# Performance work log

Hardware: AMD Instinct MI355X
Metric: run time of the kernel (lower is better)

Reference implementation:

```python
import jax, jax.numpy as jnp
import numpy as np

# The 8 structuring elements from the torch module, in order.
_KERNELS = np.array([
    [[1.,1.,1.],[1.,1.,1.],[1.,1.,1.]],
    [[0.,1.,1.],[0.,1.,1.],[0.,1.,1.]],
    [[1.,1.,1.],[1.,1.,1.],[0.,0.,0.]],
    [[0.,0.,0.],[0.,1.,1.],[0.,1.,1.]],
    [[0.,1.,0.],[0.,1.,0.],[0.,1.,0.]],
    [[0.,0.,0.],[1.,1.,1.],[0.,0.,0.]],
    [[0.,1.,0.],[0.,1.,0.],[0.,0.,0.]],
    [[0.,0.,0.],[1.,1.,0.],[0.,0.,0.]],
], dtype=np.float32)


def _conv3x3(x, k):
    # x: [N,1,H,W], k: [3,3] -> same-padded single-channel conv (cross-correlation, like torch conv2d)
    return jax.lax.conv_general_dilated(
        x, k[None, None, :, :], window_strides=(1, 1),
        padding=((1, 1), (1, 1)),
        dimension_numbers=('NCHW', 'OIHW', 'NCHW'))


def setup_inputs() -> dict:
    key = jax.random.key(0)
    N, H, W = 16, 1024, 1024
    x = (jax.random.uniform(key, (N, 1, H, W)) < 0.5).astype(jnp.float32)
    kernels = jnp.asarray(_KERNELS)  # [8,3,3]
    return {"x": x, "kernels": kernels}


def reference(x, kernels):
    output = jnp.zeros_like(x)
    # Sequential loop over the 8 fixed structuring elements (data dependency on x).
    for i in range(8):
        k = kernels[i]
        eroded = _conv3x3(x, k)
        ksum = jnp.sum(k)
        mask = (eroded >= ksum).astype(x.dtype)
        output = jnp.maximum(output, mask)
        # mark(): dilate the mask with the flipped binarized kernel
        dil_k = jnp.flip((k > 0).astype(x.dtype), axis=(0, 1))
        visited = (_conv3x3(mask, dil_k) > 0).astype(x.dtype)
        x = x - visited
    # return_single_point=True branch
    sp = _conv3x3(output, kernels[0])
    output = jnp.where((sp > 0) & (sp < 2), jnp.ones_like(sp), jnp.zeros_like(sp))
    return output
```

## Files before the change

### kernel.cpp

```cpp
#include <hip/hip_runtime.h>
#include <stdint.h>


typedef unsigned long long u64;

#define WIDTH   1024
#define HEIGHT  1024
#define NIMG    16
#define WPR     16
#define TH      64
#define PR      98
#define PW      18
#define NTHR    512

__global__ __launch_bounds__(256) void pack_kernel(const float* __restrict__ x,
                                                   u64* __restrict__ packed) {
    int rowg = blockIdx.x;
    int tid  = threadIdx.x;
    int wv   = tid >> 6;
    int lane = tid & 63;
    const float* base = x + (size_t)rowg * WIDTH + wv * 256;
    u64* pbase = packed + (size_t)rowg * WPR + wv * 4;
    #pragma unroll
    for (int j = 0; j < 4; ++j) {
        float f = base[j * 64 + lane];
        u64 m = __ballot(f > 0.5f);
        if (lane == 0) pbase[j] = m;
    }
}

template <int CM>
__device__ __forceinline__ u64 hand(const u64* Ar, int w) {
    u64 c = Ar[w], res = ~0ULL;
    if (CM & 2) res &= c;
    if (CM & 1) res &= (c << 1) | (Ar[w - 1] >> 63);
    if (CM & 4) res &= (c >> 1) | (Ar[w + 1] << 63);
    return res;
}
template <int CM>
__device__ __forceinline__ u64 hor(const u64* Ar, int w) {
    u64 c = Ar[w], res = 0;
    if (CM & 2) res |= c;
    if (CM & 1) res |= (c >> 1) | (Ar[w + 1] << 63);
    if (CM & 4) res |= (c << 1) | (Ar[w - 1] >> 63);
    return res;
}
template <int RM>
__device__ __forceinline__ u64 vand(const u64 (*A)[PW], int r, int w) {
    u64 res = ~0ULL;
    if (RM & 1) res &= A[r - 1][w];
    if (RM & 2) res &= A[r][w];
    if (RM & 4) res &= A[r + 1][w];
    return res;
}
template <int RM>
__device__ __forceinline__ u64 vor(const u64 (*A)[PW], int r, int w) {
    u64 res = 0;
    if (RM & 1) res |= A[r + 1][w];
    if (RM & 2) res |= A[r][w];
    if (RM & 4) res |= A[r - 1][w];
    return res;
}

template <int R, typename F>
__device__ __forceinline__ void forcells(F f) {
    for (int idx = threadIdx.x; idx < (TH + 2 * R) * WPR; idx += NTHR) {
        int r = 17 - R + (idx >> 4);
        int w = 1 + (idx & 15);
        f(r, w);
    }
    __syncthreads();
}

template <int RM, int CM, int HR, int MR, int DHR, int BR, bool DIL>
__device__ __forceinline__ void morph_step(u64 (&B)[PR][PW], u64 (&T)[PR][PW],
                                           u64 (&M)[PR][PW], u64 (&O)[PR][PW]) {
    if (CM != 2 && RM != 2) {
        forcells<HR>([&](int r, int w) { T[r][w] = hand<CM>(B[r], w); });
        forcells<MR>([&](int r, int w) {
            u64 m = vand<RM>(T, r, w); M[r][w] = m; O[r][w] |= m;
        });
    } else if (CM == 2) {
        forcells<MR>([&](int r, int w) {
            u64 m = vand<RM>(B, r, w); M[r][w] = m; O[r][w] |= m;
        });
    } else {
        forcells<MR>([&](int r, int w) {
            u64 m = hand<CM>(B[r], w); M[r][w] = m; O[r][w] |= m;
        });
    }
    if (DIL) {
        if (CM != 2 && RM != 2) {
            forcells<DHR>([&](int r, int w) { T[r][w] = hor<CM>(M[r], w); });
            forcells<BR>([&](int r, int w) { B[r][w] &= ~vor<RM>(T, r, w); });
        } else if (CM == 2) {
            forcells<BR>([&](int r, int w) { B[r][w] &= ~vor<RM>(M, r, w); });
        } else {
            forcells<BR>([&](int r, int w) { B[r][w] &= ~hor<CM>(M[r], w); });
        }
    }
}

__global__ __launch_bounds__(NTHR) void morph_kernel(const u64* __restrict__ packed,
                                                     float* __restrict__ out) {
    __shared__ u64 B[PR][PW];
    __shared__ u64 T[PR][PW];
    __shared__ u64 M[PR][PW];
    __shared__ u64 O[PR][PW];
    int tid = threadIdx.x;
    int ty = blockIdx.x, img = blockIdx.y;

    {
        u64* bf = &B[0][0]; u64* mf = &M[0][0]; u64* of = &O[0][0];
        for (int i = tid; i < PR * PW; i += NTHR) { bf[i] = 0; mf[i] = 0; of[i] = 0; }
    }
    __syncthreads();

    const u64* pimg = packed + (size_t)img * HEIGHT * WPR;
    for (int idx = tid; idx < (TH + 32) * WPR; idx += NTHR) {
        int rr = idx >> 4, w = idx & 15;
        int gy = ty * TH - 16 + rr;
        if (gy >= 0 && gy < HEIGHT)
            B[rr + 1][w + 1] = pimg[(size_t)gy * WPR + w];
    }
    __syncthreads();

    morph_step<7, 7, 16, 15, 15, 14, true >(B, T, M, O);
    morph_step<7, 6, 14, 13, 13, 12, true >(B, T, M, O);
    morph_step<3, 7, 12, 11, 11, 10, true >(B, T, M, O);
    morph_step<6, 6, 10,  9,  9,  8, true >(B, T, M, O);
    morph_step<7, 2,  8,  7,  7,  6, true >(B, T, M, O);
    morph_step<2, 7,  6,  5,  5,  4, true >(B, T, M, O);
    morph_step<3, 2,  4,  3,  3,  2, true >(B, T, M, O);
    morph_step<2, 3,  2,  1,  1,  0, false>(B, T, M, O);

    forcells<0>([&](int r, int w) {
        u64 ones = 0;
        u64 twos = 0;
        #pragma unroll
        for (int dr = -1; dr <= 1; ++dr) {
            const u64* Ar = O[r + dr];
            u64 c  = Ar[w];
            u64 wv = (c << 1) | (Ar[w - 1] >> 63);
            u64 ev = (c >> 1) | (Ar[w + 1] << 63);
            twos |= ones & wv; ones ^= wv;
            twos |= ones & c;  ones ^= c;
            twos |= ones & ev; ones ^= ev;
        }
        T[r][w] = ones & ~twos;
    });

    float* obase = out + ((size_t)img * HEIGHT + (size_t)ty * TH) * WIDTH;
    for (int idx = tid; idx < TH * (WIDTH / 4); idx += NTHR) {
        int row = idx >> 8;
        int q   = idx & 255;
        u64 word = T[17 + row][1 + (q >> 4)];
        int b = (q & 15) * 4;
        float4 v;
        v.x = (float)((word >> (b + 0)) & 1ULL);
        v.y = (float)((word >> (b + 1)) & 1ULL);
        v.z = (float)((word >> (b + 2)) & 1ULL);
        v.w = (float)((word >> (b + 3)) & 1ULL);
        *(float4*)(obase + (size_t)row * WIDTH + q * 4) = v;
    }
}

extern "C" void kernel_launch(void* const* d_in, const int* in_sizes, int n_in,
                              void* d_out, int out_size, void* d_ws, size_t ws_size,
                              hipStream_t stream) {
    const float* x = (const float*)d_in[0];
    float* out = (float*)d_out;
    u64* packed = (u64*)d_ws;

    hipLaunchKernelGGL(pack_kernel, dim3(NIMG * HEIGHT), dim3(256), 0, stream, x, packed);
    hipLaunchKernelGGL(morph_kernel, dim3(HEIGHT / TH, NIMG), dim3(NTHR), 0, stream,
                       packed, out);
}
```

Before: 125.9 us.

## Halve morph tile height, vectorize bit packing, and use nontemporal output stores

The pack kernel now has each wave handle a full row, reading float4 vectors and merging nibbles through xor-shuffles, so loads are wider and each block packs four rows. The morph kernel tile height drops from 64 to 32 rows while keeping the 16-row halo. That gives twice as many blocks and a smaller shared-memory footprint, which should raise occupancy, but the halo recompute overhead doubles relative to useful rows. Output stores become nontemporal so the streamed result does not pollute the cache.

```diff
diff --git a/kernel.cpp b/kernel.cpp
--- a/kernel.cpp
+++ b/kernel.cpp
@@ -3,29 +3,37 @@
 
 
 typedef unsigned long long u64;
+typedef float vfloat4 __attribute__((ext_vector_type(4)));
 
 #define WIDTH   1024
 #define HEIGHT  1024
 #define NIMG    16
 #define WPR     16
-#define TH      64
-#define PR      98
+#define TH      32
+#define HALO    16
+#define RRROWS  64
+#define PR      66
 #define PW      18
 #define NTHR    512
+#define PACK_ROWS 4
 
 __global__ __launch_bounds__(256) void pack_kernel(const float* __restrict__ x,
                                                    u64* __restrict__ packed) {
-    int rowg = blockIdx.x;
-    int tid  = threadIdx.x;
-    int wv   = tid >> 6;
-    int lane = tid & 63;
-    const float* base = x + (size_t)rowg * WIDTH + wv * 256;
-    u64* pbase = packed + (size_t)rowg * WPR + wv * 4;
+    int wv = threadIdx.x >> 6, lane = threadIdx.x & 63;
+    int row = blockIdx.x * PACK_ROWS + wv;
+    const float* rbase = x + (size_t)row * WIDTH;
+    u64* pbase = packed + (size_t)row * WPR;
     #pragma unroll
-    for (int j = 0; j < 4; ++j) {
-        float f = base[j * 64 + lane];
-        u64 m = __ballot(f > 0.5f);
-        if (lane == 0) pbase[j] = m;
+    for (int rnd = 0; rnd < 4; ++rnd) {
+        vfloat4 v = *(const vfloat4*)(rbase + rnd * 256 + lane * 4);
+        unsigned nib = (v.x > 0.5f ? 1u : 0u) | (v.y > 0.5f ? 2u : 0u)
+                     | (v.z > 0.5f ? 4u : 0u) | (v.w > 0.5f ? 8u : 0u);
+        u64 n = (u64)nib << (4 * (lane & 15));
+        n |= __shfl_xor(n, 1);
+        n |= __shfl_xor(n, 2);
+        n |= __shfl_xor(n, 4);
+        n |= __shfl_xor(n, 8);
+        if ((lane & 15) == 0) pbase[rnd * 4 + (lane >> 4)] = n;
     }
 }
 
@@ -117,9 +125,9 @@
     __syncthreads();
 
     const u64* pimg = packed + (size_t)img * HEIGHT * WPR;
-    for (int idx = tid; idx < (TH + 32) * WPR; idx += NTHR) {
+    for (int idx = tid; idx < RRROWS * WPR; idx += NTHR) {
         int rr = idx >> 4, w = idx & 15;
-        int gy = ty * TH - 16 + rr;
+        int gy = ty * TH - HALO + rr;
         if (gy >= 0 && gy < HEIGHT)
             B[rr + 1][w + 1] = pimg[(size_t)gy * WPR + w];
     }
@@ -156,12 +164,12 @@
         int q   = idx & 255;
         u64 word = T[17 + row][1 + (q >> 4)];
         int b = (q & 15) * 4;
-        float4 v;
+        vfloat4 v;
         v.x = (float)((word >> (b + 0)) & 1ULL);
         v.y = (float)((word >> (b + 1)) & 1ULL);
         v.z = (float)((word >> (b + 2)) & 1ULL);
         v.w = (float)((word >> (b + 3)) & 1ULL);
-        *(float4*)(obase + (size_t)row * WIDTH + q * 4) = v;
+        __builtin_nontemporal_store(v, (vfloat4*)(obase + (size_t)row * WIDTH + q * 4));
     }
 }
 
@@ -172,7 +180,8 @@
     float* out = (float*)d_out;
     u64* packed = (u64*)d_ws;
 
-    hipLaunchKernelGGL(pack_kernel, dim3(NIMG * HEIGHT), dim3(256), 0, stream, x, packed);
+    hipLaunchKernelGGL(pack_kernel, dim3(NIMG * HEIGHT / PACK_ROWS), dim3(256), 0,
+                       stream, x, packed);
     hipLaunchKernelGGL(morph_kernel, dim3(HEIGHT / TH, NIMG), dim3(NTHR), 0, stream,
                        packed, out);
 }
```

New measurement: 117.4 us. 1.07x faster.
